# Performance work log

Hardware: AMD Instinct MI355X
Metric: run time of the kernel (lower is better)

## Reference

```python
import jax, jax.numpy as jnp
import numpy as np

EPS = 1e-5  # torch BatchNorm default eps

def _bn(x, gamma, beta, axes):
    # training-mode batch norm: biased batch statistics over `axes`
    mean = jnp.mean(x, axis=axes, keepdims=True)
    var = jnp.var(x, axis=axes, keepdims=True)
    return gamma * (x - mean) / jnp.sqrt(var + EPS) + beta

def setup_inputs() -> dict:
    key = jax.random.key(0)
    ks = jax.random.split(key, 8)
    q, k, h, w, d, F = 64, 256, 8, 8, 512, 2048
    S = h * w  # seq_len = 64
    tgt = jax.random.normal(ks[0], (q, h, w, d), jnp.float32)
    memory = jax.random.normal(ks[1], (k, h, w, d), jnp.float32)
    W1 = jax.random.normal(ks[2], (d, d), jnp.float32) * 0.02
    b1 = jnp.zeros((d,), jnp.float32)
    se = jax.random.normal(ks[3], (S, S), jnp.float32)
    score_embed = (se + se.T).reshape(1, 1, S, S)  # symmetric, as in __init__
    W2 = jax.random.normal(ks[4], (F, S), jnp.float32) * 0.02
    b2 = jnp.zeros((F,), jnp.float32)
    W3 = jax.random.normal(ks[5], (1, F), jnp.float32) * 0.02
    b3 = jnp.zeros((1,), jnp.float32)
    g1 = jnp.ones((1,), jnp.float32); be1 = jnp.zeros((1,), jnp.float32)
    g2 = jnp.ones((F,), jnp.float32); be2 = jnp.zeros((F,), jnp.float32)
    g3 = jnp.ones((1,), jnp.float32); be3 = jnp.zeros((1,), jnp.float32)
    return dict(tgt=tgt, memory=memory, W1=W1, b1=b1, score_embed=score_embed,
                W2=W2, b2=b2, W3=W3, b3=b3,
                g1=g1, be1=be1, g2=g2, be2=be2, g3=g3, be3=be3, flag=1)

def reference(tgt, memory, W1, b1, score_embed, W2, b2, W3, b3,
              g1, be1, g2, be2, g3, be3, flag):
    q, h, w, d = tgt.shape
    kk = memory.shape[0]
    S = h * w
    tgt_f = tgt.reshape(q, S, d)
    mem_f = memory.reshape(kk, S, d)
    if flag:
        query = tgt_f @ W1.T + b1
        keym = mem_f @ W1.T + b1
        # [q, k, s, t] score tensor modulated by learned symmetric embedding
        score = jnp.einsum('qtd,ksd->qkst', query, keym) * jax.nn.sigmoid(score_embed)
    else:
        score = jnp.einsum('qtd,ksd->qkst', tgt_f, mem_f)
    score = score.reshape(q * kk, S, S)
    # dual-axis max pooling over score map, concatenated -> [q*k, 2S]
    score = jnp.concatenate([score.max(axis=1), score.max(axis=2)], axis=-1)
    x = score.reshape(-1, 1, S)                     # [2qk, 1, S]
    x = _bn(x, g1.reshape(1, 1, 1), be1.reshape(1, 1, 1), (0, 2)).reshape(-1, S)
    x = x @ W2.T + b2                               # [2qk, F]
    x = jax.nn.relu(_bn(x, g2, be2, (0,)))
    x = x @ W3.T + b3                               # [2qk, 1]
    x = x.reshape(-1, 2).sum(axis=-1, keepdims=True)  # [qk, 1]
    x = _bn(x, g3, be3, (0,))
    return x.reshape(q, kk)
```

## Files before the change

kernel.cpp:

```cpp
#include <hip/hip_runtime.h>
#include <hip/hip_bf16.h>
#include <math.h>
#include <float.h>

constexpr int NQ = 64, NK = 256, SSZ = 64, D = 512, FF = 2048;
constexpr int PAIRS = NQ * NK;
constexpr int ROWSX = 2 * PAIRS;
constexpr int NX = (NQ + NK) * SSZ;
constexpr int SBLK = 128;

typedef __bf16 bf16x8 __attribute__((ext_vector_type(8)));
typedef float floatx16 __attribute__((ext_vector_type(16)));

__device__ __forceinline__ void gl2lds16(const unsigned short* g, unsigned short* l) {
    __builtin_amdgcn_global_load_lds(
        (const __attribute__((address_space(1))) unsigned int*)(g),
        (__attribute__((address_space(3))) unsigned int*)(l),
        16, 0, 0);
}


__global__ void k_sig(const float* __restrict__ se, const int* __restrict__ flag,
                      float* __restrict__ sig) {
    int i = blockIdx.x * blockDim.x + threadIdx.x;
    if (i < SSZ * SSZ) {
        sig[i] = (*flag) ? 1.0f / (1.0f + expf(-se[i])) : 1.0f;
    }
}

__global__ __launch_bounds__(256) void k_cvt(
        const float* __restrict__ tgt, const float* __restrict__ mem,
        const float* __restrict__ W1, const float* __restrict__ W2,
        __hip_bfloat16* __restrict__ Xb, __hip_bfloat16* __restrict__ W1b,
        __hip_bfloat16* __restrict__ W2b) {
    constexpr int T4 = NQ * SSZ * D / 4;
    constexpr int X4 = NX * D / 4;
    constexpr int W4 = D * D / 4;
    constexpr int V4 = FF * 64 / 4;
    int idx = blockIdx.x * 256 + threadIdx.x;
    if (idx >= X4 + W4 + V4) return;
    const float* src;
    __hip_bfloat16* dst;
    if (idx < T4)           { src = tgt + (size_t)idx * 4;             dst = Xb + (size_t)idx * 4; }
    else if (idx < X4)      { src = mem + (size_t)(idx - T4) * 4;      dst = Xb + (size_t)idx * 4; }
    else if (idx < X4 + W4) { src = W1 + (size_t)(idx - X4) * 4;       dst = W1b + (size_t)(idx - X4) * 4; }
    else                    { src = W2 + (size_t)(idx - X4 - W4) * 4;  dst = W2b + (size_t)(idx - X4 - W4) * 4; }
    float4 v = *reinterpret_cast<const float4*>(src);
    union { __hip_bfloat16 h[4]; uint2 u; } o;
    o.h[0] = __float2bfloat16(v.x); o.h[1] = __float2bfloat16(v.y);
    o.h[2] = __float2bfloat16(v.z); o.h[3] = __float2bfloat16(v.w);
    *reinterpret_cast<uint2*>(dst) = o.u;
}

__global__ __launch_bounds__(256, 3) void k_gemm1_mfma(
        const __hip_bfloat16* __restrict__ Xb, const __hip_bfloat16* __restrict__ W1b,
        const float* __restrict__ b1, const int* __restrict__ flag,
        __hip_bfloat16* __restrict__ QKf) {
    __shared__ __attribute__((aligned(16))) unsigned short lds[2 * 128 * 64];
    const unsigned short* Xu = reinterpret_cast<const unsigned short*>(Xb);
    const unsigned short* Wu = reinterpret_cast<const unsigned short*>(W1b);
    unsigned short* Fu = reinterpret_cast<unsigned short*>(QKf);

    int tid = threadIdx.x;
    int bm = blockIdx.x >> 2, bn = blockIdx.x & 3;
    int m0 = bm * 128, n0 = bn * 128;

    if (!(*flag)) {
#pragma unroll
        for (int i = 0; i < 8; ++i) {
            int e = i * 256 + tid;
            int fb = e >> 6;
            int lp = e & 63;
            int rgl = fb >> 3, kgl = fb & 7;
            int row = m0 + rgl * 32 + (lp & 31);
            int col = n0 + kgl * 16 + (lp >> 5) * 8;
            uint4 v = *reinterpret_cast<const uint4*>(Xu + (size_t)row * D + col);
            size_t ofs = ((size_t)((m0 >> 5) + rgl) * 32 + (n0 >> 4) + kgl) * 512 + lp * 8;
            *reinterpret_cast<uint4*>(Fu + ofs) = v;
        }
        return;
    }

    int w = tid >> 6, l = tid & 63, h = l >> 5, c = l & 31;
    int wm = w >> 1, wn = w & 1;
    int chg = (l & 7) ^ (l >> 3);
    int cx = c & 7;
    floatx16 acc00 = {}, acc01 = {}, acc10 = {}, acc11 = {};

    for (int kb = 0; kb < D; kb += 64) {
#pragma unroll
        for (int j = 0; j < 8; ++j) {
            int i = w * 8 + j;
            int buf = i >> 4;
            int rb = (i & 15) * 8;
            int r = rb + (l >> 3);
            const unsigned short* src = (buf == 0)
                ? (Xu + (size_t)(m0 + r) * D + kb + chg * 8)
                : (Wu + (size_t)(n0 + r) * D + kb + chg * 8);
            gl2lds16(src, lds + buf * 8192 + rb * 64);
        }
        __syncthreads();
        const unsigned short* pA = lds + (wm * 64) * 64;
        const unsigned short* pB = lds + 8192 + (wn * 64) * 64;
#pragma unroll
        for (int st = 0; st < 4; ++st) {
            int ko = ((st * 2 + h) ^ cx) * 8;
            bf16x8 a0 = *reinterpret_cast<const bf16x8*>(pA + c * 64 + ko);
            bf16x8 a1 = *reinterpret_cast<const bf16x8*>(pA + (32 + c) * 64 + ko);
            bf16x8 b0 = *reinterpret_cast<const bf16x8*>(pB + c * 64 + ko);
            bf16x8 b1v = *reinterpret_cast<const bf16x8*>(pB + (32 + c) * 64 + ko);
            acc00 = __builtin_amdgcn_mfma_f32_32x32x16_bf16(b0, a0, acc00, 0, 0, 0);
            acc01 = __builtin_amdgcn_mfma_f32_32x32x16_bf16(b0, a1, acc01, 0, 0, 0);
            acc10 = __builtin_amdgcn_mfma_f32_32x32x16_bf16(b1v, a0, acc10, 0, 0, 0);
            acc11 = __builtin_amdgcn_mfma_f32_32x32x16_bf16(b1v, a1, acc11, 0, 0, 0);
        }
        __syncthreads();
    }

#pragma unroll
    for (int ni = 0; ni < 2; ++ni) {
        int nb = n0 + wn * 64 + ni * 32;
#pragma unroll
        for (int mi = 0; mi < 2; ++mi) {
            const floatx16& A = ni ? (mi ? acc11 : acc10) : (mi ? acc01 : acc00);
            int mb = m0 + wm * 64 + mi * 32;
            size_t rgbase = ((size_t)(mb >> 5) * 32 + (nb >> 4)) * 512;
#pragma unroll
            for (int g = 0; g < 4; ++g) {
                float4 bia = *reinterpret_cast<const float4*>(&b1[nb + 8 * g + 4 * h]);
                union { __hip_bfloat16 hh[4]; uint2 u; } o;
                o.hh[0] = __float2bfloat16(A[4 * g + 0] + bia.x);
                o.hh[1] = __float2bfloat16(A[4 * g + 1] + bia.y);
                o.hh[2] = __float2bfloat16(A[4 * g + 2] + bia.z);
                o.hh[3] = __float2bfloat16(A[4 * g + 3] + bia.w);
                *reinterpret_cast<uint2*>(Fu + rgbase + (size_t)(g >> 1) * 512
                                          + (c + 32 * (g & 1)) * 8 + 4 * h) = o.u;
            }
        }
    }
}

__global__ __launch_bounds__(512, 2) void k_score_mfma(
        const __hip_bfloat16* __restrict__ QKf, const float* __restrict__ sig,
        float* __restrict__ xbuf) {
    __shared__ __attribute__((aligned(16))) unsigned short lds[65536];
    const unsigned short* Fu = reinterpret_cast<const unsigned short*>(QKf);

    int tid = threadIdx.x;
    int w = tid >> 6, l = tid & 63, h = l >> 5, c = l & 31;
    int qig = blockIdx.x >> 5, ktg = blockIdx.x & 31;
    int kt = ktg * 8 + w;

    const unsigned short* Qg = Fu + (size_t)qig * 65536;
#pragma unroll
    for (int i = 0; i < 16; ++i) {
        int e = i * 512 + tid;
        gl2lds16(Qg + e * 8, lds + e * 8);
    }

    const unsigned short* pK0 = Fu + (size_t)(128 + kt * 2) * 16384 + l * 8;
    const unsigned short* pK1 = pK0 + 16384;

    floatx16 acc[2][4] = {};
    bf16x8 ka0[2][4], ka1[2][4];
#pragma unroll
    for (int st = 0; st < 4; ++st) {
        ka0[0][st] = *reinterpret_cast<const bf16x8*>(pK0 + st * 512);
        ka1[0][st] = *reinterpret_cast<const bf16x8*>(pK1 + st * 512);
    }
    __syncthreads();

    const unsigned short* qlds = lds + l * 8;
#pragma unroll
    for (int kbi = 0; kbi < 8; ++kbi) {
        const int cur = kbi & 1, nxt = cur ^ 1;
        if (kbi < 7) {
            pK0 += 2048; pK1 += 2048;
#pragma unroll
            for (int st = 0; st < 4; ++st) {
                ka0[nxt][st] = *reinterpret_cast<const bf16x8*>(pK0 + st * 512);
                ka1[nxt][st] = *reinterpret_cast<const bf16x8*>(pK1 + st * 512);
            }
        }
#pragma unroll
        for (int g = 0; g < 4; ++g) {
            bf16x8 qb[4];
#pragma unroll
            for (int st = 0; st < 4; ++st)
                qb[st] = *reinterpret_cast<const bf16x8*>(qlds + (g * 32 + kbi * 4 + st) * 512);
            __builtin_amdgcn_s_setprio(1);
#pragma unroll
            for (int st = 0; st < 4; ++st) {
                acc[0][g] = __builtin_amdgcn_mfma_f32_32x32x16_bf16(ka0[cur][st], qb[st], acc[0][g], 0, 0, 0);
                acc[1][g] = __builtin_amdgcn_mfma_f32_32x32x16_bf16(ka1[cur][st], qb[st], acc[1][g], 0, 0, 0);
            }
            __builtin_amdgcn_s_setprio(0);
        }
    }

    const float* sigl = sig;

    int p0 = (qig * 2) * 256 + kt;
    int p1 = p0 + 256;
    float tmax[4] = {-FLT_MAX, -FLT_MAX, -FLT_MAX, -FLT_MAX};
#pragma unroll
    for (int sh = 0; sh < 2; ++sh) {
        float smA[16], smB[16];
#pragma unroll
        for (int r = 0; r < 16; ++r) {
            int srow = sh * 32 + (r & 3) + 8 * (r >> 2) + 4 * h;
            float s0 = sigl[srow * 64 + c];
            float s1 = sigl[srow * 64 + 32 + c];
            float v0 = acc[sh][0][r] * s0;
            float v1 = acc[sh][1][r] * s1;
            float v2 = acc[sh][2][r] * s0;
            float v3 = acc[sh][3][r] * s1;
            tmax[0] = fmaxf(tmax[0], v0);
            tmax[1] = fmaxf(tmax[1], v1);
            tmax[2] = fmaxf(tmax[2], v2);
            tmax[3] = fmaxf(tmax[3], v3);
            smA[r] = fmaxf(v0, v1);
            smB[r] = fmaxf(v2, v3);
        }
#pragma unroll
        for (int stage = 1; stage < 32; stage <<= 1)
#pragma unroll
            for (int r = 0; r < 16; ++r) {
                smA[r] = fmaxf(smA[r], __shfl_xor(smA[r], stage, 64));
                smB[r] = fmaxf(smB[r], __shfl_xor(smB[r], stage, 64));
            }
        if (c == 0) {
#pragma unroll
            for (int r = 0; r < 16; ++r) {
                int srow = sh * 32 + (r & 3) + 8 * (r >> 2) + 4 * h;
                xbuf[(size_t)(2 * p0 + 1) * 64 + srow] = smA[r];
                xbuf[(size_t)(2 * p1 + 1) * 64 + srow] = smB[r];
            }
        }
    }
#pragma unroll
    for (int g = 0; g < 4; ++g)
        tmax[g] = fmaxf(tmax[g], __shfl_xor(tmax[g], 32, 64));
    if (h == 0) {
        xbuf[(size_t)(2 * p0) * 64 + c] = tmax[0];
        xbuf[(size_t)(2 * p0) * 64 + 32 + c] = tmax[1];
        xbuf[(size_t)(2 * p1) * 64 + c] = tmax[2];
        xbuf[(size_t)(2 * p1) * 64 + 32 + c] = tmax[3];
    }
}

__global__ __launch_bounds__(256) void k_stats1(const float* __restrict__ xbuf,
        float* __restrict__ S1p, float* __restrict__ S2p) {
    __shared__ float xr[8][64];
    int tid = threadIdx.x;
    int row0 = blockIdx.x * 256;
    float acc[16] = {};
    float s1 = 0.f;
    int a = tid >> 2;
    int bbase = (tid & 3) * 16;
    int lr = tid >> 5, lc = (tid & 31) * 2;
    for (int it = 0; it < 32; ++it) {
        int r = row0 + it * 8;
        *reinterpret_cast<float2*>(&xr[lr][lc]) =
            *reinterpret_cast<const float2*>(&xbuf[(size_t)(r + lr) * 64 + lc]);
        __syncthreads();
        float xa[8];
#pragma unroll
        for (int j = 0; j < 8; ++j) xa[j] = xr[j][a];
#pragma unroll
        for (int j = 0; j < 8; ++j) {
            const float4* pb = reinterpret_cast<const float4*>(&xr[j][bbase]);
            float4 b0 = pb[0], b1 = pb[1], b2 = pb[2], b3 = pb[3];
            acc[0] += xa[j] * b0.x;  acc[1] += xa[j] * b0.y;
            acc[2] += xa[j] * b0.z;  acc[3] += xa[j] * b0.w;
            acc[4] += xa[j] * b1.x;  acc[5] += xa[j] * b1.y;
            acc[6] += xa[j] * b1.z;  acc[7] += xa[j] * b1.w;
            acc[8] += xa[j] * b2.x;  acc[9] += xa[j] * b2.y;
            acc[10] += xa[j] * b2.z; acc[11] += xa[j] * b2.w;
            acc[12] += xa[j] * b3.x; acc[13] += xa[j] * b3.y;
            acc[14] += xa[j] * b3.z; acc[15] += xa[j] * b3.w;
        }
        if (tid < 64) {
#pragma unroll
            for (int j = 0; j < 8; ++j) s1 += xr[j][tid];
        }
        __syncthreads();
    }
    float* dst = S2p + (size_t)blockIdx.x * 4096 + tid * 16;
#pragma unroll
    for (int e = 0; e < 16; e += 4)
        *reinterpret_cast<float4*>(dst + e) = make_float4(acc[e], acc[e+1], acc[e+2], acc[e+3]);
    if (tid < 64) S1p[blockIdx.x * 64 + tid] = s1;
}

__global__ __launch_bounds__(256) void k_red(const float* __restrict__ S1p,
        const float* __restrict__ S2p, float* __restrict__ S1f,
        float* __restrict__ S2f) {
    int idx = blockIdx.x * 256 + threadIdx.x;
    double s = 0.0;
    for (int b = 0; b < SBLK; ++b) s += (double)S2p[(size_t)b * 4096 + idx];
    S2f[idx] = (float)s;
    if (blockIdx.x == 0 && threadIdx.x < 64) {
        double s1 = 0.0;
        for (int b = 0; b < SBLK; ++b) s1 += (double)S1p[b * 64 + threadIdx.x];
        S1f[threadIdx.x] = (float)s1;
    }
}

__global__ __launch_bounds__(256) void k_fin1(
        const float* __restrict__ S1f, const float* __restrict__ S2f,
        const float* __restrict__ g1, const float* __restrict__ be1,
        float* __restrict__ bn1, float* __restrict__ xbarn, float* __restrict__ covn) {
    int tid = threadIdx.x;
    double sum = 0.0, sumsq = 0.0;
    for (int j = 0; j < 64; ++j) { sum += (double)S1f[j]; sumsq += (double)S2f[j * 65]; }
    const double Nall = (double)ROWSX * 64.0;
    double m1 = sum / Nall;
    double var1 = sumsq / Nall - m1 * m1;
    double scaled = (double)g1[0] / sqrt(var1 + 1e-5);
    if (tid == 0) { bn1[0] = (float)m1; bn1[1] = (float)scaled; }
    const double Rinv = 1.0 / (double)ROWSX;
    if (tid < 64) xbarn[tid] = (float)(((double)S1f[tid] * Rinv - m1) * scaled) + be1[0];
#pragma unroll
    for (int e = 0; e < 16; ++e) {
        int idx = tid * 16 + e;
        int a = idx >> 6, b = idx & 63;
        double cov = (double)S2f[idx] * Rinv
                   - ((double)S1f[a] * Rinv) * ((double)S1f[b] * Rinv);
        covn[idx] = (float)(cov * scaled * scaled);
    }
}

__global__ __launch_bounds__(256) void k_bn2(
        const float* __restrict__ covn, const float* __restrict__ xbarn,
        const __hip_bfloat16* __restrict__ W2b,
        const float* __restrict__ g2, const float* __restrict__ be2,
        float* __restrict__ alpha, float* __restrict__ beta) {
    int w = threadIdx.x >> 6;
    int j = threadIdx.x & 63;
    int f = blockIdx.x * 4 + w;
    float wj = __bfloat162float(W2b[(size_t)f * 64 + j]);
    float t1 = 0.f;
    for (int b = 0; b < 64; ++b)
        t1 += covn[j * 64 + b] * __bfloat162float(W2b[(size_t)f * 64 + b]);
    float vc = wj * t1;
    float mc = wj * xbarn[j];
#pragma unroll
    for (int off = 32; off; off >>= 1) {
        vc += __shfl_down(vc, off);
        mc += __shfl_down(mc, off);
    }
    if (j == 0) {
        float t2 = g2[f] * rsqrtf(vc + 1e-5f);
        alpha[f] = t2;
        beta[f] = -t2 * mc + be2[f];
    }
}

__global__ __launch_bounds__(256, 4) void k_mlp_mfma(
        const float* __restrict__ xbuf, const float* __restrict__ bn1,
        const float* __restrict__ be1, const __hip_bfloat16* __restrict__ W2b,
        const float* __restrict__ alpha, const float* __restrict__ beta,
        const float* __restrict__ W3, const float* __restrict__ b3,
        float* __restrict__ z) {
    constexpr int LDR = 72;
    __shared__ __attribute__((aligned(16))) unsigned short Xs[128 * LDR];
    __shared__ __attribute__((aligned(16))) unsigned short Ws[128 * LDR];
    __shared__ float abw[3 * 128];
    const unsigned short* W2u = reinterpret_cast<const unsigned short*>(W2b);
    int tid = threadIdx.x;
    int w = tid >> 6, l = tid & 63, h = l >> 5, c = l & 31;
    int r0 = blockIdx.x * 128;
    float m1 = bn1[0], sc = bn1[1], sh = be1[0];

#pragma unroll
    for (int i = 0; i < 4; ++i) {
        int id = i * 256 + tid;
        int row = id >> 3, cg = id & 7;
        const float* src = xbuf + (size_t)(r0 + row) * 64 + cg * 8;
        float4 v0 = *reinterpret_cast<const float4*>(src);
        float4 v1 = *reinterpret_cast<const float4*>(src + 4);
        union { __hip_bfloat16 hh[8]; uint4 u; } o;
        o.hh[0] = __float2bfloat16((v0.x - m1) * sc + sh);
        o.hh[1] = __float2bfloat16((v0.y - m1) * sc + sh);
        o.hh[2] = __float2bfloat16((v0.z - m1) * sc + sh);
        o.hh[3] = __float2bfloat16((v0.w - m1) * sc + sh);
        o.hh[4] = __float2bfloat16((v1.x - m1) * sc + sh);
        o.hh[5] = __float2bfloat16((v1.y - m1) * sc + sh);
        o.hh[6] = __float2bfloat16((v1.z - m1) * sc + sh);
        o.hh[7] = __float2bfloat16((v1.w - m1) * sc + sh);
        *reinterpret_cast<uint4*>(&Xs[row * LDR + cg * 8]) = o.u;
    }

    float zacc[16] = {};
    for (int fc = 0; fc < FF / 128; ++fc) {
#pragma unroll
        for (int i = 0; i < 4; ++i) {
            int id = i * 256 + tid;
            int row = id >> 3, cg = id & 7;
            uint4 v = *reinterpret_cast<const uint4*>(W2u + (size_t)(fc * 128 + row) * 64 + cg * 8);
            *reinterpret_cast<uint4*>(&Ws[row * LDR + cg * 8]) = v;
        }
        if (tid < 128) {
            int f = fc * 128 + tid;
            abw[tid] = alpha[f];
            abw[128 + tid] = beta[f];
            abw[256 + tid] = W3[f];
        }
        __syncthreads();
        bf16x8 a[4];
#pragma unroll
        for (int st = 0; st < 4; ++st)
            a[st] = *reinterpret_cast<const bf16x8*>(&Xs[(w * 32 + c) * LDR + st * 16 + h * 8]);
#pragma unroll
        for (int nq = 0; nq < 4; ++nq) {
            floatx16 u = {};
#pragma unroll
            for (int st = 0; st < 4; ++st) {
                bf16x8 b = *reinterpret_cast<const bf16x8*>(&Ws[(nq * 32 + c) * LDR + st * 16 + h * 8]);
                u = __builtin_amdgcn_mfma_f32_32x32x16_bf16(a[st], b, u, 0, 0, 0);
            }
            float al = abw[nq * 32 + c];
            float bt = abw[128 + nq * 32 + c];
            float w3 = abw[256 + nq * 32 + c];
#pragma unroll
            for (int r = 0; r < 16; ++r)
                zacc[r] += fmaxf(al * u[r] + bt, 0.f) * w3;
        }
        __syncthreads();
    }
#pragma unroll
    for (int stage = 1; stage < 32; stage <<= 1)
#pragma unroll
        for (int r = 0; r < 16; ++r)
            zacc[r] += __shfl_xor(zacc[r], stage, 64);
    if (c == 0) {
        float bb = b3[0];
#pragma unroll
        for (int r = 0; r < 16; ++r) {
            int row = r0 + w * 32 + (r & 3) + 8 * (r >> 2) + 4 * h;
            z[row] = zacc[r] + bb;
        }
    }
}

__global__ __launch_bounds__(256) void k_pair(const float* __restrict__ z,
        float* __restrict__ v, double* __restrict__ sums3) {
    int i = blockIdx.x * 256 + threadIdx.x;
    float val = z[2 * i] + z[2 * i + 1];
    v[i] = val;
    float s = val, ss = val * val;
#pragma unroll
    for (int off = 32; off; off >>= 1) {
        s += __shfl_down(s, off);
        ss += __shfl_down(ss, off);
    }
    __shared__ float bs[4], bss[4];
    int lane = threadIdx.x & 63, w = threadIdx.x >> 6;
    if (lane == 0) { bs[w] = s; bss[w] = ss; }
    __syncthreads();
    if (threadIdx.x == 0) {
        atomicAdd(&sums3[0], (double)(bs[0] + bs[1] + bs[2] + bs[3]));
        atomicAdd(&sums3[1], (double)(bss[0] + bss[1] + bss[2] + bss[3]));
    }
}

__global__ void k_fin3(const double* __restrict__ sums3, const float* __restrict__ g3,
                       float* __restrict__ bn3) {
    double m = sums3[0] / (double)PAIRS;
    double var = sums3[1] / (double)PAIRS - m * m;
    bn3[0] = (float)m;
    bn3[1] = (float)((double)g3[0] / sqrt(var + 1e-5));
}

__global__ void k_out(const float* __restrict__ v, const float* __restrict__ bn3,
                      const float* __restrict__ be3, float* __restrict__ out) {
    int i = blockIdx.x * 256 + threadIdx.x;
    if (i < PAIRS) out[i] = (v[i] - bn3[0]) * bn3[1] + be3[0];
}

extern "C" void kernel_launch(void* const* d_in, const int* in_sizes, int n_in,
                              void* d_out, int out_size, void* d_ws, size_t ws_size,
                              hipStream_t stream) {
    (void)in_sizes; (void)n_in; (void)out_size; (void)ws_size;
    const float* tgt = (const float*)d_in[0];
    const float* mem = (const float*)d_in[1];
    const float* W1  = (const float*)d_in[2];
    const float* b1  = (const float*)d_in[3];
    const float* se  = (const float*)d_in[4];
    const float* W2  = (const float*)d_in[5];
    const float* b2  = (const float*)d_in[6];
    const float* W3  = (const float*)d_in[7];
    const float* b3  = (const float*)d_in[8];
    const float* g1  = (const float*)d_in[9];
    const float* be1 = (const float*)d_in[10];
    const float* g2  = (const float*)d_in[11];
    const float* be2 = (const float*)d_in[12];
    const float* g3  = (const float*)d_in[13];
    const float* be3 = (const float*)d_in[14];
    const int*  flag = (const int*)d_in[15];
    (void)b2;
    float* out = (float*)d_out;

    char* ws = (char*)d_ws;
    size_t off = 0;
    auto alloc = [&](size_t bytes) -> void* {
        void* p = ws + off;
        off = (off + bytes + 255) & ~(size_t)255;
        return p;
    };
    float* sig   = (float*)alloc((size_t)SSZ * SSZ * 4);
    __hip_bfloat16* Xb  = (__hip_bfloat16*)alloc((size_t)NX * D * 2);
    __hip_bfloat16* W1b = (__hip_bfloat16*)alloc((size_t)D * D * 2);
    __hip_bfloat16* W2b = (__hip_bfloat16*)alloc((size_t)FF * 64 * 2);
    __hip_bfloat16* QKf = (__hip_bfloat16*)alloc((size_t)NX * D * 2);
    float* xbuf  = (float*)alloc((size_t)ROWSX * 64 * 4);
    float* z     = (float*)alloc((size_t)ROWSX * 4);
    float* v     = (float*)alloc((size_t)PAIRS * 4);
    float* alpha = (float*)alloc((size_t)FF * 4);
    float* beta  = (float*)alloc((size_t)FF * 4);
    float* xbarn = (float*)alloc(64 * 4);
    float* covn  = (float*)alloc(64 * 64 * 4);
    float* bn1   = (float*)alloc(16);
    float* bn3   = (float*)alloc(16);
    float* S1p   = (float*)alloc((size_t)SBLK * 64 * 4);
    float* S2p   = (float*)alloc((size_t)SBLK * 4096 * 4);
    float* S1f   = (float*)alloc(64 * 4);
    float* S2f   = (float*)alloc(4096 * 4);
    size_t statsStart = off;
    double* sums3 = (double*)alloc(2 * 8);
    size_t statsEnd = off;

    hipMemsetAsync(ws + statsStart, 0, statsEnd - statsStart, stream);

    k_sig<<<16, 256, 0, stream>>>(se, flag, sig);
    constexpr int CVT4 = (NX * D + D * D + FF * 64) / 4;
    k_cvt<<<(CVT4 + 255) / 256, 256, 0, stream>>>(tgt, mem, W1, W2, Xb, W1b, W2b);
    k_gemm1_mfma<<<(NX / 128) * (D / 128), 256, 0, stream>>>(Xb, W1b, b1, flag, QKf);
    k_score_mfma<<<(NQ / 2) * (NK / 8), 512, 0, stream>>>(QKf, sig, xbuf);
    k_stats1<<<SBLK, 256, 0, stream>>>(xbuf, S1p, S2p);
    k_red<<<16, 256, 0, stream>>>(S1p, S2p, S1f, S2f);
    k_fin1<<<1, 256, 0, stream>>>(S1f, S2f, g1, be1, bn1, xbarn, covn);
    k_bn2<<<FF / 4, 256, 0, stream>>>(covn, xbarn, W2b, g2, be2, alpha, beta);
    k_mlp_mfma<<<ROWSX / 128, 256, 0, stream>>>(xbuf, bn1, be1, W2b, alpha, beta, W3, b3, z);
    k_pair<<<PAIRS / 256, 256, 0, stream>>>(z, v, sums3);
    k_fin3<<<1, 1, 0, stream>>>(sums3, g3, bn3);
    k_out<<<PAIRS / 256, 256, 0, stream>>>(v, bn3, be3, out);
}
```

Measured before the change: 298.7 us.

## Fold small finalize kernels into neighbors to cut launch count

Merges the sigmoid kernel into the conversion kernel, drops k_fin1 by recomputing BN1 statistics and covariance terms inside k_bn2 and k_mlp_mfma, and folds k_fin3 into k_out. k_red is also widened to 64 blocks, each splitting its reduction over four thread groups. The goal is to remove three tiny serial launches and the gaps between them, and to parallelise the reduction. The cost is redundant per-block recomputation of the scalar statistics, and the covariance normalisation now runs in float instead of double.

```diff
diff --git a/kernel.cpp b/kernel.cpp
--- a/kernel.cpp
+++ b/kernel.cpp
@@ -20,25 +20,31 @@
 }
 
 
-__global__ void k_sig(const float* __restrict__ se, const int* __restrict__ flag,
-                      float* __restrict__ sig) {
-    int i = blockIdx.x * blockDim.x + threadIdx.x;
-    if (i < SSZ * SSZ) {
-        sig[i] = (*flag) ? 1.0f / (1.0f + expf(-se[i])) : 1.0f;
-    }
-}
-
 __global__ __launch_bounds__(256) void k_cvt(
         const float* __restrict__ tgt, const float* __restrict__ mem,
         const float* __restrict__ W1, const float* __restrict__ W2,
+        const float* __restrict__ se, const int* __restrict__ flag,
         __hip_bfloat16* __restrict__ Xb, __hip_bfloat16* __restrict__ W1b,
-        __hip_bfloat16* __restrict__ W2b) {
+        __hip_bfloat16* __restrict__ W2b, float* __restrict__ sig) {
     constexpr int T4 = NQ * SSZ * D / 4;
     constexpr int X4 = NX * D / 4;
     constexpr int W4 = D * D / 4;
     constexpr int V4 = FF * 64 / 4;
+    constexpr int S4 = SSZ * SSZ / 4;
     int idx = blockIdx.x * 256 + threadIdx.x;
-    if (idx >= X4 + W4 + V4) return;
+    if (idx >= X4 + W4 + V4 + S4) return;
+    if (idx >= X4 + W4 + V4) {
+        int s = (idx - X4 - W4 - V4) * 4;
+        float4 v = *reinterpret_cast<const float4*>(se + s);
+        bool fl = (*flag) != 0;
+        float4 o;
+        o.x = fl ? 1.0f / (1.0f + expf(-v.x)) : 1.0f;
+        o.y = fl ? 1.0f / (1.0f + expf(-v.y)) : 1.0f;
+        o.z = fl ? 1.0f / (1.0f + expf(-v.z)) : 1.0f;
+        o.w = fl ? 1.0f / (1.0f + expf(-v.w)) : 1.0f;
+        *reinterpret_cast<float4*>(sig + s) = o;
+        return;
+    }
     const float* src;
     __hip_bfloat16* dst;
     if (idx < T4)           { src = tgt + (size_t)idx * 4;             dst = Xb + (size_t)idx * 4; }
@@ -296,55 +302,68 @@
 __global__ __launch_bounds__(256) void k_red(const float* __restrict__ S1p,
         const float* __restrict__ S2p, float* __restrict__ S1f,
         float* __restrict__ S2f) {
-    int idx = blockIdx.x * 256 + threadIdx.x;
+    __shared__ double part[4][64];
+    int tid = threadIdx.x;
+    int il = tid & 63, bq = tid >> 6;
+    int idx = blockIdx.x * 64 + il;
     double s = 0.0;
-    for (int b = 0; b < SBLK; ++b) s += (double)S2p[(size_t)b * 4096 + idx];
-    S2f[idx] = (float)s;
-    if (blockIdx.x == 0 && threadIdx.x < 64) {
+    for (int b = bq * 32; b < bq * 32 + 32; ++b)
+        s += (double)S2p[(size_t)b * 4096 + idx];
+    part[bq][il] = s;
+    __syncthreads();
+    if (tid < 64) {
+        double t = part[0][tid] + part[1][tid] + part[2][tid] + part[3][tid];
+        S2f[blockIdx.x * 64 + tid] = (float)t;
+    }
+    if (blockIdx.x == 0 && tid >= 64 && tid < 128) {
+        int j = tid - 64;
         double s1 = 0.0;
-        for (int b = 0; b < SBLK; ++b) s1 += (double)S1p[b * 64 + threadIdx.x];
-        S1f[threadIdx.x] = (float)s1;
-    }
-}
-
-__global__ __launch_bounds__(256) void k_fin1(
+        for (int b = 0; b < SBLK; ++b) s1 += (double)S1p[b * 64 + j];
+        S1f[j] = (float)s1;
+    }
+}
+
+__global__ __launch_bounds__(256) void k_bn2(
         const float* __restrict__ S1f, const float* __restrict__ S2f,
+        const __hip_bfloat16* __restrict__ W2b,
         const float* __restrict__ g1, const float* __restrict__ be1,
-        float* __restrict__ bn1, float* __restrict__ xbarn, float* __restrict__ covn) {
-    int tid = threadIdx.x;
-    double sum = 0.0, sumsq = 0.0;
-    for (int j = 0; j < 64; ++j) { sum += (double)S1f[j]; sumsq += (double)S2f[j * 65]; }
-    const double Nall = (double)ROWSX * 64.0;
-    double m1 = sum / Nall;
-    double var1 = sumsq / Nall - m1 * m1;
-    double scaled = (double)g1[0] / sqrt(var1 + 1e-5);
-    if (tid == 0) { bn1[0] = (float)m1; bn1[1] = (float)scaled; }
-    const double Rinv = 1.0 / (double)ROWSX;
-    if (tid < 64) xbarn[tid] = (float)(((double)S1f[tid] * Rinv - m1) * scaled) + be1[0];
-#pragma unroll
-    for (int e = 0; e < 16; ++e) {
-        int idx = tid * 16 + e;
-        int a = idx >> 6, b = idx & 63;
-        double cov = (double)S2f[idx] * Rinv
-                   - ((double)S1f[a] * Rinv) * ((double)S1f[b] * Rinv);
-        covn[idx] = (float)(cov * scaled * scaled);
-    }
-}
-
-__global__ __launch_bounds__(256) void k_bn2(
-        const float* __restrict__ covn, const float* __restrict__ xbarn,
-        const __hip_bfloat16* __restrict__ W2b,
         const float* __restrict__ g2, const float* __restrict__ be2,
         float* __restrict__ alpha, float* __restrict__ beta) {
-    int w = threadIdx.x >> 6;
-    int j = threadIdx.x & 63;
+    __shared__ float mb[64];
+    __shared__ float scal[3];
+    int tid = threadIdx.x;
+    const float Rinvf = 1.0f / (float)ROWSX;
+    if (tid < 64) {
+        double ss = (double)S1f[tid];
+        double sq = (double)S2f[tid * 65];
+#pragma unroll
+        for (int off = 32; off; off >>= 1) {
+            ss += __shfl_down(ss, off);
+            sq += __shfl_down(sq, off);
+        }
+        if (tid == 0) {
+            const double Nall = (double)ROWSX * 64.0;
+            double m1 = ss / Nall;
+            double var1 = sq / Nall - m1 * m1;
+            double scaled = (double)g1[0] / sqrt(var1 + 1e-5);
+            scal[0] = (float)(scaled * scaled);
+            scal[1] = (float)m1;
+            scal[2] = (float)scaled;
+        }
+        mb[tid] = S1f[tid] * Rinvf;
+    }
+    __syncthreads();
+    int w = tid >> 6;
+    int j = tid & 63;
     int f = blockIdx.x * 4 + w;
     float wj = __bfloat162float(W2b[(size_t)f * 64 + j]);
+    float mj = mb[j];
     float t1 = 0.f;
     for (int b = 0; b < 64; ++b)
-        t1 += covn[j * 64 + b] * __bfloat162float(W2b[(size_t)f * 64 + b]);
-    float vc = wj * t1;
-    float mc = wj * xbarn[j];
+        t1 += (S2f[j * 64 + b] * Rinvf - mj * mb[b]) * __bfloat162float(W2b[(size_t)f * 64 + b]);
+    float vc = wj * t1 * scal[0];
+    float xbj = (mj - scal[1]) * scal[2] + be1[0];
+    float mc = wj * xbj;
 #pragma unroll
     for (int off = 32; off; off >>= 1) {
         vc += __shfl_down(vc, off);
@@ -358,7 +377,8 @@
 }
 
 __global__ __launch_bounds__(256, 4) void k_mlp_mfma(
-        const float* __restrict__ xbuf, const float* __restrict__ bn1,
+        const float* __restrict__ xbuf, const float* __restrict__ S1f,
+        const float* __restrict__ S2f, const float* __restrict__ g1,
         const float* __restrict__ be1, const __hip_bfloat16* __restrict__ W2b,
         const float* __restrict__ alpha, const float* __restrict__ beta,
         const float* __restrict__ W3, const float* __restrict__ b3,
@@ -367,11 +387,30 @@
     __shared__ __attribute__((aligned(16))) unsigned short Xs[128 * LDR];
     __shared__ __attribute__((aligned(16))) unsigned short Ws[128 * LDR];
     __shared__ float abw[3 * 128];
+    __shared__ float scl[2];
     const unsigned short* W2u = reinterpret_cast<const unsigned short*>(W2b);
     int tid = threadIdx.x;
     int w = tid >> 6, l = tid & 63, h = l >> 5, c = l & 31;
     int r0 = blockIdx.x * 128;
-    float m1 = bn1[0], sc = bn1[1], sh = be1[0];
+
+    if (tid < 64) {
+        double ss = (double)S1f[tid];
+        double sq = (double)S2f[tid * 65];
+#pragma unroll
+        for (int off = 32; off; off >>= 1) {
+            ss += __shfl_down(ss, off);
+            sq += __shfl_down(sq, off);
+        }
+        if (tid == 0) {
+            const double Nall = (double)ROWSX * 64.0;
+            double m1 = ss / Nall;
+            double var1 = sq / Nall - m1 * m1;
+            scl[0] = (float)m1;
+            scl[1] = (float)((double)g1[0] / sqrt(var1 + 1e-5));
+        }
+    }
+    __syncthreads();
+    float m1 = scl[0], sc = scl[1], sh = be1[0];
 
 #pragma unroll
     for (int i = 0; i < 4; ++i) {
@@ -465,18 +504,15 @@
     }
 }
 
-__global__ void k_fin3(const double* __restrict__ sums3, const float* __restrict__ g3,
-                       float* __restrict__ bn3) {
+__global__ __launch_bounds__(256) void k_out(const float* __restrict__ v,
+        const double* __restrict__ sums3, const float* __restrict__ g3,
+        const float* __restrict__ be3, float* __restrict__ out) {
     double m = sums3[0] / (double)PAIRS;
     double var = sums3[1] / (double)PAIRS - m * m;
-    bn3[0] = (float)m;
-    bn3[1] = (float)((double)g3[0] / sqrt(var + 1e-5));
-}
-
-__global__ void k_out(const float* __restrict__ v, const float* __restrict__ bn3,
-                      const float* __restrict__ be3, float* __restrict__ out) {
+    float mm = (float)m;
+    float inv = (float)((double)g3[0] / sqrt(var + 1e-5));
     int i = blockIdx.x * 256 + threadIdx.x;
-    if (i < PAIRS) out[i] = (v[i] - bn3[0]) * bn3[1] + be3[0];
+    if (i < PAIRS) out[i] = (v[i] - mm) * inv + be3[0];
 }
 
 extern "C" void kernel_launch(void* const* d_in, const int* in_sizes, int n_in,
@@ -519,10 +555,6 @@
     float* v     = (float*)alloc((size_t)PAIRS * 4);
     float* alpha = (float*)alloc((size_t)FF * 4);
     float* beta  = (float*)alloc((size_t)FF * 4);
-    float* xbarn = (float*)alloc(64 * 4);
-    float* covn  = (float*)alloc(64 * 64 * 4);
-    float* bn1   = (float*)alloc(16);
-    float* bn3   = (float*)alloc(16);
     float* S1p   = (float*)alloc((size_t)SBLK * 64 * 4);
     float* S2p   = (float*)alloc((size_t)SBLK * 4096 * 4);
     float* S1f   = (float*)alloc(64 * 4);
@@ -533,17 +565,17 @@
 
     hipMemsetAsync(ws + statsStart, 0, statsEnd - statsStart, stream);
 
-    k_sig<<<16, 256, 0, stream>>>(se, flag, sig);
     constexpr int CVT4 = (NX * D + D * D + FF * 64) / 4;
-    k_cvt<<<(CVT4 + 255) / 256, 256, 0, stream>>>(tgt, mem, W1, W2, Xb, W1b, W2b);
+    constexpr int SIG4 = SSZ * SSZ / 4;
+    k_cvt<<<(CVT4 + SIG4 + 255) / 256, 256, 0, stream>>>(
+        tgt, mem, W1, W2, se, flag, Xb, W1b, W2b, sig);
     k_gemm1_mfma<<<(NX / 128) * (D / 128), 256, 0, stream>>>(Xb, W1b, b1, flag, QKf);
     k_score_mfma<<<(NQ / 2) * (NK / 8), 512, 0, stream>>>(QKf, sig, xbuf);
     k_stats1<<<SBLK, 256, 0, stream>>>(xbuf, S1p, S2p);
-    k_red<<<16, 256, 0, stream>>>(S1p, S2p, S1f, S2f);
-    k_fin1<<<1, 256, 0, stream>>>(S1f, S2f, g1, be1, bn1, xbarn, covn);
-    k_bn2<<<FF / 4, 256, 0, stream>>>(covn, xbarn, W2b, g2, be2, alpha, beta);
-    k_mlp_mfma<<<ROWSX / 128, 256, 0, stream>>>(xbuf, bn1, be1, W2b, alpha, beta, W3, b3, z);
+    k_red<<<64, 256, 0, stream>>>(S1p, S2p, S1f, S2f);
+    k_bn2<<<FF / 4, 256, 0, stream>>>(S1f, S2f, W2b, g1, be1, g2, be2, alpha, beta);
+    k_mlp_mfma<<<ROWSX / 128, 256, 0, stream>>>(xbuf, S1f, S2f, g1, be1, W2b,
+                                                alpha, beta, W3, b3, z);
     k_pair<<<PAIRS / 256, 256, 0, stream>>>(z, v, sums3);
-    k_fin3<<<1, 1, 0, stream>>>(sums3, g3, bn3);
-    k_out<<<PAIRS / 256, 256, 0, stream>>>(v, bn3, be3, out);
-}
+    k_out<<<PAIRS / 256, 256, 0, stream>>>(v, sums3, g3, be3, out);
+}
```

Measured after the change: 293.0 us. Within noise of the previous version (-1.9%).
